# Performance work log

Hardware: AMD Instinct MI355X
Metric: run time of the kernel (lower is better)

The kernel has to match this reference:

```python
import jax, jax.numpy as jnp
import numpy as np

B, L, D = 8, 4096, 768
EPS = 1e-5


def layer_norm(x, g, b):
    mu = jnp.mean(x, axis=-1, keepdims=True)
    var = jnp.mean(jnp.square(x - mu), axis=-1, keepdims=True)
    return (x - mu) * jax.lax.rsqrt(var + EPS) * g + b


def conv1d_same(x_blc, w_oik, b_o):
    # x_blc: [B, L, C] -> torch Conv1d(C, C, 3, padding=1) on [B, C, L]
    x_ncw = jnp.swapaxes(x_blc, 1, 2)
    y = jax.lax.conv_general_dilated(
        x_ncw, w_oik, window_strides=(1,), padding=[(1, 1)],
        dimension_numbers=("NCW", "OIW", "NCW"))
    y = y + b_o[None, :, None]
    return jnp.swapaxes(y, 1, 2)


def simple_ssm(u, a_p, b_p, c_p, d_p):
    # Diagonal SSM: h_t = sigmoid(a)*h_{t-1} + b*u_t ; y_t = c*h_t + d*u_t
    a = jax.nn.sigmoid(a_p)  # [D]

    def step(h, ut):  # h, ut: [B, D]
        h = a * h + b_p * ut
        return h, c_p * h

    h0 = jnp.zeros((u.shape[0], u.shape[2]), u.dtype)
    _, y = jax.lax.scan(step, h0, jnp.swapaxes(u, 0, 1))  # y: [L, B, D]
    return jnp.swapaxes(y, 0, 1) + d_p * u


def setup_inputs() -> dict:
    key = jax.random.key(0)
    ks = jax.random.split(key, 16)
    s_lin = 1.0 / np.sqrt(D)
    s_conv = 1.0 / np.sqrt(3 * D)
    return {
        "x": jax.random.normal(ks[0], (B, L, D), jnp.float32),
        "ln_g": jnp.ones((D,), jnp.float32),
        "ln_b": jnp.zeros((D,), jnp.float32),
        "Wi": jax.random.normal(ks[1], (D, 2 * D), jnp.float32) * s_lin,
        "bi": jnp.zeros((2 * D,), jnp.float32),
        "Wf_conv": jax.random.normal(ks[2], (D, D, 3), jnp.float32) * s_conv,
        "bf_conv": jnp.zeros((D,), jnp.float32),
        "af": jax.random.normal(ks[3], (D,), jnp.float32),
        "bf": jax.random.normal(ks[4], (D,), jnp.float32) * 0.5,
        "cf": jax.random.normal(ks[5], (D,), jnp.float32) * 0.5,
        "df": jax.random.normal(ks[6], (D,), jnp.float32) * 0.5,
        "Wb_conv": jax.random.normal(ks[7], (D, D, 3), jnp.float32) * s_conv,
        "bb_conv": jnp.zeros((D,), jnp.float32),
        "ab": jax.random.normal(ks[8], (D,), jnp.float32),
        "bb": jax.random.normal(ks[9], (D,), jnp.float32) * 0.5,
        "cb": jax.random.normal(ks[10], (D,), jnp.float32) * 0.5,
        "db": jax.random.normal(ks[11], (D,), jnp.float32) * 0.5,
        "Wo": jax.random.normal(ks[12], (D, D), jnp.float32) * s_lin,
        "bo": jnp.zeros((D,), jnp.float32),
    }


def reference(x, ln_g, ln_b, Wi, bi, Wf_conv, bf_conv, af, bf, cf, df,
              Wb_conv, bb_conv, ab, bb, cb, db, Wo, bo):
    residual = x
    xn = layer_norm(x, ln_g, ln_b)
    proj = xn @ Wi + bi                      # [B, L, 2D]
    xg, z = proj[..., :D], proj[..., D:]
    # forward branch
    f = conv1d_same(xg, Wf_conv, bf_conv)
    f = simple_ssm(f, af, bf, cf, df)
    # backward branch (flip along sequence)
    b_in = jnp.flip(xg, axis=1)
    bb_out = conv1d_same(b_in, Wb_conv, bb_conv)
    bb_out = simple_ssm(bb_out, ab, bb, cb, db)
    bb_out = jnp.flip(bb_out, axis=1)
    zg = jax.nn.silu(z)
    y = f * zg + bb_out * zg
    return y @ Wo + bo + residual
```

## Files before the change

### kernel.cpp

```cpp
#include <hip/hip_runtime.h>
#include <cstdint>
#include <cstddef>
#include <math.h>

#define L_SEQ 4096
#define D_DIM 768
#define B_SZ 8
#define M_ROWS (B_SZ * L_SEQ)
#define CHUNK 64

typedef __bf16 bf16x8 __attribute__((ext_vector_type(8)));
typedef float floatx4 __attribute__((ext_vector_type(4)));

#define GLP(p)  ((__attribute__((address_space(1))) const void*)(const void*)(p))
#define LDSP(p) ((__attribute__((address_space(3))) void*)(void*)(p))

__global__ __launch_bounds__(256) void ln_kernel(const float* __restrict__ x,
                                                 const float* __restrict__ g,
                                                 const float* __restrict__ b,
                                                 __bf16* __restrict__ xn) {
  __shared__ float red[256];
  const int tid = threadIdx.x;
  const size_t row = blockIdx.x;
  const float* xr = x + row * D_DIM;
  float v0 = xr[tid];
  float v1 = xr[tid + 256];
  float v2 = xr[tid + 512];
  red[tid] = v0 + v1 + v2;
  __syncthreads();
  for (int off = 128; off > 0; off >>= 1) {
    if (tid < off) red[tid] += red[tid + off];
    __syncthreads();
  }
  float mu = red[0] * (1.0f / D_DIM);
  __syncthreads();
  float d0 = v0 - mu, d1 = v1 - mu, d2 = v2 - mu;
  red[tid] = d0 * d0 + d1 * d1 + d2 * d2;
  __syncthreads();
  for (int off = 128; off > 0; off >>= 1) {
    if (tid < off) red[tid] += red[tid + off];
    __syncthreads();
  }
  float rs = rsqrtf(red[0] * (1.0f / D_DIM) + 1e-5f);
  __bf16* xo = xn + row * D_DIM;
  xo[tid]       = (__bf16)(d0 * rs * g[tid]       + b[tid]);
  xo[tid + 256] = (__bf16)(d1 * rs * g[tid + 256] + b[tid + 256]);
  xo[tid + 512] = (__bf16)(d2 * rs * g[tid + 512] + b[tid + 512]);
}

template<int MODE>
__global__ __launch_bounds__(256) void gemm_kernel(
    const __bf16* __restrict__ A,
    const __bf16* __restrict__ Bt,
    const float* __restrict__ bias,
    const float* __restrict__ resid,
    __bf16* __restrict__ out0,
    __bf16* __restrict__ out1,
    float* __restrict__ outf,
    const __bf16* __restrict__ zbuf,
    int K) {
  __shared__ __bf16 As[128 * 32];
  __shared__ __bf16 Bs[128 * 32];
  const int tid   = threadIdx.x;
  const int tileN = blockIdx.x;
  const int tileM = blockIdx.y;
  const int lane = tid & 63;
  const int w    = tid >> 6;
  const int wm   = w >> 1;
  const int wn   = w & 1;
  const int l15  = lane & 15;
  const int quad = lane >> 4;
  const int colg = (lane & 3) * 8;
  const int rsub = lane >> 2;

  const int rowA0 = w * 32 + rsub;
  const int rowA1 = rowA0 + 16;

  const __bf16* gB0 = Bt + (size_t)(tileN * 128 + rowA0) * K + colg;
  const __bf16* gB1 = Bt + (size_t)(tileN * 128 + rowA1) * K + colg;

  const __bf16* gA0 = nullptr;
  const __bf16* gA1 = nullptr;
  int bl0 = 0, bl1 = 0, l0 = 0, l1 = 0;
  if (MODE == 1 || MODE == 2) {
    int gr0 = tileM * 128 + rowA0;
    int gr1 = tileM * 128 + rowA1;
    bl0 = gr0 >> 12; l0 = gr0 & (L_SEQ - 1);
    bl1 = gr1 >> 12; l1 = gr1 & (L_SEQ - 1);
  } else {
    gA0 = A + (size_t)(tileM * 128 + rowA0) * K + colg;
    gA1 = A + (size_t)(tileM * 128 + rowA1) * K + colg;
  }

  __bf16* ldsA0 = &As[(w * 32) * 32];
  __bf16* ldsA1 = &As[(w * 32 + 16) * 32];
  __bf16* ldsB0 = &Bs[(w * 32) * 32];
  __bf16* ldsB1 = &Bs[(w * 32 + 16) * 32];

  floatx4 acc[4][4];
#pragma unroll
  for (int i = 0; i < 4; ++i)
#pragma unroll
    for (int j = 0; j < 4; ++j)
#pragma unroll
      for (int r = 0; r < 4; ++r) acc[i][j][r] = 0.0f;

  int kblk = 0, i0 = 0;
  for (int kt = 0; kt < K; kt += 32) {
    __syncthreads();
    const __bf16* pa0;
    const __bf16* pa1;
    if (MODE == 1 || MODE == 2) {
      int ls0 = (MODE == 1) ? (l0 + kblk - 1) : (L_SEQ - l0 - kblk);
      int ls1 = (MODE == 1) ? (l1 + kblk - 1) : (L_SEQ - l1 - kblk);
      pa0 = (ls0 >= 0 && ls0 < L_SEQ)
          ? A + ((size_t)(bl0 << 12) + (size_t)ls0) * D_DIM + i0 + colg : zbuf;
      pa1 = (ls1 >= 0 && ls1 < L_SEQ)
          ? A + ((size_t)(bl1 << 12) + (size_t)ls1) * D_DIM + i0 + colg : zbuf;
    } else {
      pa0 = gA0 + kt;
      pa1 = gA1 + kt;
    }
    __builtin_amdgcn_global_load_lds(GLP(pa0), LDSP(ldsA0), 16, 0, 0);
    __builtin_amdgcn_global_load_lds(GLP(pa1), LDSP(ldsA1), 16, 0, 0);
    __builtin_amdgcn_global_load_lds(GLP(gB0 + kt), LDSP(ldsB0), 16, 0, 0);
    __builtin_amdgcn_global_load_lds(GLP(gB1 + kt), LDSP(ldsB1), 16, 0, 0);
    __syncthreads();

    bf16x8 afr[4], bfr[4];
#pragma unroll
    for (int i = 0; i < 4; ++i)
      afr[i] = *(const bf16x8*)(&As[(wm * 64 + i * 16 + l15) * 32 + quad * 8]);
#pragma unroll
    for (int j = 0; j < 4; ++j)
      bfr[j] = *(const bf16x8*)(&Bs[(wn * 64 + j * 16 + l15) * 32 + quad * 8]);
#pragma unroll
    for (int i = 0; i < 4; ++i)
#pragma unroll
      for (int j = 0; j < 4; ++j)
        acc[i][j] = __builtin_amdgcn_mfma_f32_16x16x32_bf16(afr[i], bfr[j], acc[i][j], 0, 0, 0);

    i0 += 32;
    if (i0 == D_DIM) { i0 = 0; ++kblk; }
  }

#pragma unroll
  for (int i = 0; i < 4; ++i) {
#pragma unroll
    for (int j = 0; j < 4; ++j) {
#pragma unroll
      for (int r = 0; r < 4; ++r) {
        int row = tileM * 128 + wm * 64 + i * 16 + quad * 4 + r;
        int col = tileN * 128 + wn * 64 + j * 16 + l15;
        float v = acc[i][j][r] + bias[col];
        if (MODE == 0) {
          if (col < D_DIM) {
            out0[(size_t)row * D_DIM + col] = (__bf16)v;
          } else {
            float s = v / (1.0f + expf(-v));
            out1[(size_t)row * D_DIM + (col - D_DIM)] = (__bf16)s;
          }
        } else if (MODE == 3) {
          size_t o = (size_t)row * D_DIM + col;
          outf[o] = v + resid[o];
        } else {
          out0[(size_t)row * D_DIM + col] = (__bf16)v;
        }
      }
    }
  }
}

__global__ __launch_bounds__(256) void scan1_kernel(
    const float* __restrict__ ap0, const float* __restrict__ bp0,
    const float* __restrict__ ap1, const float* __restrict__ bp1,
    const __bf16* __restrict__ u0, const __bf16* __restrict__ u1,
    float* __restrict__ hl) {
  int idx = blockIdx.x * 256 + threadIdx.x;
  int d = idx % D_DIM;
  int rest = idx / D_DIM;
  int chunk = rest & 63;
  int tb = rest >> 6;
  int b = tb & 7;
  int tensor = tb >> 3;
  const float* ap = tensor ? ap1 : ap0;
  const float* bp = tensor ? bp1 : bp0;
  const __bf16* u = (tensor ? u1 : u0) +
      ((size_t)(b * L_SEQ + chunk * CHUNK)) * D_DIM + d;
  float a  = 1.0f / (1.0f + expf(-ap[d]));
  float bb = bp[d];
  float h = 0.0f;
  for (int t = 0; t < CHUNK; ++t) {
    h = a * h + bb * (float)u[(size_t)t * D_DIM];
  }
  hl[(size_t)idx] = h;
}

__global__ __launch_bounds__(256) void scan2_kernel(
    const float* __restrict__ ap0, const float* __restrict__ ap1,
    float* __restrict__ hl) {
  int idx = blockIdx.x * 256 + threadIdx.x;
  int d = idx % D_DIM;
  int tb = idx / D_DIM;
  int tensor = tb >> 3;
  const float* ap = tensor ? ap1 : ap0;
  float a = 1.0f / (1.0f + expf(-ap[d]));
  float aT = a * a;  aT = aT * aT;  aT = aT * aT;
  aT = aT * aT;      aT = aT * aT;  aT = aT * aT;
  float* base = hl + (size_t)tb * 64 * D_DIM + d;
  float carry = 0.0f;
  for (int c = 0; c < 64; ++c) {
    float* p = base + (size_t)c * D_DIM;
    float tmp = *p;
    *p = carry;
    carry = aT * carry + tmp;
  }
}

__global__ __launch_bounds__(256) void scan3_kernel(
    const float* __restrict__ ap0, const float* __restrict__ bp0,
    const float* __restrict__ cp0, const float* __restrict__ dp0,
    const float* __restrict__ ap1, const float* __restrict__ bp1,
    const float* __restrict__ cp1, const float* __restrict__ dp1,
    __bf16* __restrict__ u0, __bf16* __restrict__ u1,
    const float* __restrict__ hl) {
  int idx = blockIdx.x * 256 + threadIdx.x;
  int d = idx % D_DIM;
  int rest = idx / D_DIM;
  int chunk = rest & 63;
  int tb = rest >> 6;
  int b = tb & 7;
  int tensor = tb >> 3;
  const float* ap = tensor ? ap1 : ap0;
  const float* bp = tensor ? bp1 : bp0;
  const float* cp = tensor ? cp1 : cp0;
  const float* dp = tensor ? dp1 : dp0;
  __bf16* u = (tensor ? u1 : u0) +
      ((size_t)(b * L_SEQ + chunk * CHUNK)) * D_DIM + d;
  float a  = 1.0f / (1.0f + expf(-ap[d]));
  float bb = bp[d];
  float cc = cp[d];
  float dd = dp[d];
  float h = hl[(size_t)idx];
  for (int t = 0; t < CHUNK; ++t) {
    float uv = (float)u[(size_t)t * D_DIM];
    h = a * h + bb * uv;
    u[(size_t)t * D_DIM] = (__bf16)(cc * h + dd * uv);
  }
}

__global__ __launch_bounds__(256) void gate_kernel(const __bf16* __restrict__ f,
                                                   const __bf16* __restrict__ bbuf,
                                                   const __bf16* __restrict__ zg,
                                                   __bf16* __restrict__ y) {
  size_t idx = (size_t)blockIdx.x * 256 + threadIdx.x;
  int d = (int)(idx % D_DIM);
  size_t rl = idx / D_DIM;
  int l = (int)(rl & (L_SEQ - 1));
  size_t b = rl >> 12;
  size_t src = ((b << 12) + (size_t)(L_SEQ - 1 - l)) * D_DIM + d;
  float v = ((float)f[idx] + (float)bbuf[src]) * (float)zg[idx];
  y[idx] = (__bf16)v;
}

__global__ __launch_bounds__(256) void tr_kernel(const float* __restrict__ in,
                                                 __bf16* __restrict__ out,
                                                 int Kdim, int Ndim) {
  int idx = blockIdx.x * 256 + threadIdx.x;
  if (idx >= Kdim * Ndim) return;
  int n = idx / Kdim;
  int k = idx - n * Kdim;
  out[idx] = (__bf16)in[(size_t)k * Ndim + n];
}

__global__ __launch_bounds__(256) void trconv_kernel(const float* __restrict__ in,
                                                     __bf16* __restrict__ out) {
  int idx = blockIdx.x * 256 + threadIdx.x;
  if (idx >= D_DIM * 2304) return;
  int o = idx / 2304;
  int rem = idx - o * 2304;
  int k = rem / D_DIM;
  int i = rem - k * D_DIM;
  out[idx] = (__bf16)in[(size_t)o * 2304 + i * 3 + k];
}

__global__ void zero_kernel(__bf16* z) { z[threadIdx.x] = (__bf16)0.0f; }

extern "C" void kernel_launch(void* const* d_in, const int* in_sizes, int n_in,
                              void* d_out, int out_size, void* d_ws, size_t ws_size,
                              hipStream_t stream) {
  const float* x    = (const float*)d_in[0];
  const float* ln_g = (const float*)d_in[1];
  const float* ln_b = (const float*)d_in[2];
  const float* Wi   = (const float*)d_in[3];
  const float* bi   = (const float*)d_in[4];
  const float* Wf   = (const float*)d_in[5];
  const float* bfc  = (const float*)d_in[6];
  const float* af   = (const float*)d_in[7];
  const float* bfp  = (const float*)d_in[8];
  const float* cfp  = (const float*)d_in[9];
  const float* dfp  = (const float*)d_in[10];
  const float* Wb   = (const float*)d_in[11];
  const float* bbc  = (const float*)d_in[12];
  const float* ab   = (const float*)d_in[13];
  const float* bbp  = (const float*)d_in[14];
  const float* cbp  = (const float*)d_in[15];
  const float* dbp  = (const float*)d_in[16];
  const float* Wo   = (const float*)d_in[17];
  const float* bo   = (const float*)d_in[18];
  float* out = (float*)d_out;

  char* ws = (char*)d_ws;
  const size_t BLD = (size_t)B_SZ * L_SEQ * D_DIM;
  __bf16* ws0 = (__bf16*)(ws);
  __bf16* ws1 = (__bf16*)(ws + BLD * 2);
  __bf16* ws2 = (__bf16*)(ws + BLD * 4);
  __bf16* ws3 = (__bf16*)(ws + BLD * 6);
  __bf16* wit = (__bf16*)(ws + BLD * 8);
  __bf16* wft = wit + (size_t)1536 * 768;
  __bf16* wbt = wft + (size_t)768 * 2304;
  __bf16* wot = wbt + (size_t)768 * 2304;
  __bf16* zbuf = wot + (size_t)768 * 768;
  float* hl = (float*)(ws + BLD * 2);
  const size_t needed = BLD * 8 +
      ((size_t)1536 * 768 + 2 * (size_t)768 * 2304 + (size_t)768 * 768) * 2 + 256;
  if (ws_size < needed) return;

  zero_kernel<<<1, 128, 0, stream>>>(zbuf);
  tr_kernel<<<(768 * 1536 + 255) / 256, 256, 0, stream>>>(Wi, wit, 768, 1536);
  trconv_kernel<<<(768 * 2304 + 255) / 256, 256, 0, stream>>>(Wf, wft);
  trconv_kernel<<<(768 * 2304 + 255) / 256, 256, 0, stream>>>(Wb, wbt);
  tr_kernel<<<(768 * 768 + 255) / 256, 256, 0, stream>>>(Wo, wot, 768, 768);

  ln_kernel<<<M_ROWS, 256, 0, stream>>>(x, ln_g, ln_b, ws0);

  gemm_kernel<0><<<dim3(1536 / 128, M_ROWS / 128), 256, 0, stream>>>(
      ws0, wit, bi, nullptr, ws1, ws2, nullptr, zbuf, 768);

  gemm_kernel<1><<<dim3(768 / 128, M_ROWS / 128), 256, 0, stream>>>(
      ws1, wft, bfc, nullptr, ws0, nullptr, nullptr, zbuf, 2304);
  gemm_kernel<2><<<dim3(768 / 128, M_ROWS / 128), 256, 0, stream>>>(
      ws1, wbt, bbc, nullptr, ws3, nullptr, nullptr, zbuf, 2304);

  {
    const int n1 = 2 * B_SZ * 64 * D_DIM;
    scan1_kernel<<<n1 / 256, 256, 0, stream>>>(af, bfp, ab, bbp, ws0, ws3, hl);
    const int n2 = 2 * B_SZ * D_DIM;
    scan2_kernel<<<n2 / 256, 256, 0, stream>>>(af, ab, hl);
    scan3_kernel<<<n1 / 256, 256, 0, stream>>>(af, bfp, cfp, dfp,
                                               ab, bbp, cbp, dbp,
                                               ws0, ws3, hl);
  }

  gate_kernel<<<(unsigned)(BLD / 256), 256, 0, stream>>>(ws0, ws3, ws2, ws1);

  gemm_kernel<3><<<dim3(768 / 128, M_ROWS / 128), 256, 0, stream>>>(
      ws1, wot, bo, x, nullptr, nullptr, out, zbuf, 768);
}
```

Measured before the change: 879.6 us.

## Replace GEMMs with 256x256 pipelined kernel, merge conv branches, vectorize scans

```diff
diff --git a/kernel.cpp b/kernel.cpp
--- a/kernel.cpp
+++ b/kernel.cpp
@@ -48,123 +48,195 @@
   xo[tid + 512] = (__bf16)(d2 * rs * g[tid + 512] + b[tid + 512]);
 }
 
-template<int MODE>
-__global__ __launch_bounds__(256) void gemm_kernel(
-    const __bf16* __restrict__ A,
-    const __bf16* __restrict__ Bt,
-    const float* __restrict__ bias,
+
+#define VMW(n) asm volatile("s_waitcnt vmcnt(" #n ")" ::: "memory")
+#define BARR   asm volatile("s_barrier" ::: "memory")
+#define MF(a, b, c) __builtin_amdgcn_mfma_f32_16x16x32_bf16((a), (b), (c), 0, 0, 0)
+#define LDV(off) (*(const bf16x8*)(smem + (off)))
+
+#define RDA(BUF, MOFF) do { \
+  aR0k0 = LDV((BUF)*65536 + aoff + (MOFF) + ck0);        aR0k1 = LDV((BUF)*65536 + aoff + (MOFF) + ck1); \
+  aR1k0 = LDV((BUF)*65536 + aoff + (MOFF) + 2048 + ck0); aR1k1 = LDV((BUF)*65536 + aoff + (MOFF) + 2048 + ck1); \
+  aR2k0 = LDV((BUF)*65536 + aoff + (MOFF) + 4096 + ck0); aR2k1 = LDV((BUF)*65536 + aoff + (MOFF) + 4096 + ck1); \
+  aR3k0 = LDV((BUF)*65536 + aoff + (MOFF) + 6144 + ck0); aR3k1 = LDV((BUF)*65536 + aoff + (MOFF) + 6144 + ck1); \
+} while (0)
+
+#define RDB01(BUF) do { \
+  bN0k0 = LDV((BUF)*65536 + boff + ck0);        bN0k1 = LDV((BUF)*65536 + boff + ck1); \
+  bN1k0 = LDV((BUF)*65536 + boff + 2048 + ck0); bN1k1 = LDV((BUF)*65536 + boff + 2048 + ck1); \
+} while (0)
+
+#define RDB23(BUF) do { \
+  bN2k0 = LDV((BUF)*65536 + boff + 4096 + ck0); bN2k1 = LDV((BUF)*65536 + boff + 4096 + ck1); \
+  bN3k0 = LDV((BUF)*65536 + boff + 6144 + ck0); bN3k1 = LDV((BUF)*65536 + boff + 6144 + ck1); \
+} while (0)
+
+#define MMQ01(AI) do { \
+  acc[(AI)+0][0] = MF(aR0k0, bN0k0, acc[(AI)+0][0]); acc[(AI)+0][0] = MF(aR0k1, bN0k1, acc[(AI)+0][0]); \
+  acc[(AI)+0][1] = MF(aR0k0, bN1k0, acc[(AI)+0][1]); acc[(AI)+0][1] = MF(aR0k1, bN1k1, acc[(AI)+0][1]); \
+  acc[(AI)+1][0] = MF(aR1k0, bN0k0, acc[(AI)+1][0]); acc[(AI)+1][0] = MF(aR1k1, bN0k1, acc[(AI)+1][0]); \
+  acc[(AI)+1][1] = MF(aR1k0, bN1k0, acc[(AI)+1][1]); acc[(AI)+1][1] = MF(aR1k1, bN1k1, acc[(AI)+1][1]); \
+  acc[(AI)+2][0] = MF(aR2k0, bN0k0, acc[(AI)+2][0]); acc[(AI)+2][0] = MF(aR2k1, bN0k1, acc[(AI)+2][0]); \
+  acc[(AI)+2][1] = MF(aR2k0, bN1k0, acc[(AI)+2][1]); acc[(AI)+2][1] = MF(aR2k1, bN1k1, acc[(AI)+2][1]); \
+  acc[(AI)+3][0] = MF(aR3k0, bN0k0, acc[(AI)+3][0]); acc[(AI)+3][0] = MF(aR3k1, bN0k1, acc[(AI)+3][0]); \
+  acc[(AI)+3][1] = MF(aR3k0, bN1k0, acc[(AI)+3][1]); acc[(AI)+3][1] = MF(aR3k1, bN1k1, acc[(AI)+3][1]); \
+} while (0)
+
+#define MMQ23(AI) do { \
+  acc[(AI)+0][2] = MF(aR0k0, bN2k0, acc[(AI)+0][2]); acc[(AI)+0][2] = MF(aR0k1, bN2k1, acc[(AI)+0][2]); \
+  acc[(AI)+0][3] = MF(aR0k0, bN3k0, acc[(AI)+0][3]); acc[(AI)+0][3] = MF(aR0k1, bN3k1, acc[(AI)+0][3]); \
+  acc[(AI)+1][2] = MF(aR1k0, bN2k0, acc[(AI)+1][2]); acc[(AI)+1][2] = MF(aR1k1, bN2k1, acc[(AI)+1][2]); \
+  acc[(AI)+1][3] = MF(aR1k0, bN3k0, acc[(AI)+1][3]); acc[(AI)+1][3] = MF(aR1k1, bN3k1, acc[(AI)+1][3]); \
+  acc[(AI)+2][2] = MF(aR2k0, bN2k0, acc[(AI)+2][2]); acc[(AI)+2][2] = MF(aR2k1, bN2k1, acc[(AI)+2][2]); \
+  acc[(AI)+2][3] = MF(aR2k0, bN3k0, acc[(AI)+2][3]); acc[(AI)+2][3] = MF(aR2k1, bN3k1, acc[(AI)+2][3]); \
+  acc[(AI)+3][2] = MF(aR3k0, bN2k0, acc[(AI)+3][2]); acc[(AI)+3][2] = MF(aR3k1, bN2k1, acc[(AI)+3][2]); \
+  acc[(AI)+3][3] = MF(aR3k0, bN3k0, acc[(AI)+3][3]); acc[(AI)+3][3] = MF(aR3k1, bN3k1, acc[(AI)+3][3]); \
+} while (0)
+
+#define STAGE_A_HP(h, p, tkt, BUF) do { \
+  const __bf16* _s; \
+  if (MODE == 1) { \
+    const int _kb = ((tkt) * 43) >> 9;                        \
+    const int _io = (((tkt) - _kb * 12) << 6) + (_kb - 1) * D_DIM; \
+    _s = ((unsigned)(lv##h##p + _kb - 1) < (unsigned)L_SEQ) ? (rb##h##p + _io) : zbuf; \
+  } else { \
+    _s = rb##h##p + (tkt) * 64; \
+  } \
+  __builtin_amdgcn_global_load_lds(GLP(_s), \
+      LDSP(smem + (BUF)*65536 + (h)*8192 + (p)*16384 + dstw), 16, 0, 0); \
+} while (0)
+
+#define STAGE_B_HP(h, p, tkt, BUF) \
+  __builtin_amdgcn_global_load_lds(GLP(pB##h##p + (tkt) * 64), \
+      LDSP(smem + (BUF)*65536 + 32768 + (h)*16384 + (p)*8192 + dstw), 16, 0, 0)
+
+#define TILE(T, BUF, VA, VC, SA1, SREST) do { \
+   \
+  VMW(VA); BARR; \
+  RDB01(BUF); RDA(BUF, 0); \
+  if (SA1) { STAGE_A_HP(1, 0, (T) + 1, (BUF) ^ 1); STAGE_A_HP(1, 1, (T) + 1, (BUF) ^ 1); } \
+  __builtin_amdgcn_s_setprio(1); MMQ01(0); __builtin_amdgcn_s_setprio(0); \
+   \
+  BARR; \
+  RDB23(BUF); \
+  if (SREST) { STAGE_A_HP(0, 0, (T) + 2, (BUF)); STAGE_A_HP(0, 1, (T) + 2, (BUF)); } \
+  __builtin_amdgcn_s_setprio(1); MMQ23(0); __builtin_amdgcn_s_setprio(0); \
+   \
+  VMW(VC); BARR; \
+  RDA(BUF, 8192); \
+  if (SREST) { STAGE_B_HP(0, 0, (T) + 2, (BUF)); STAGE_B_HP(0, 1, (T) + 2, (BUF)); } \
+  __builtin_amdgcn_s_setprio(1); MMQ01(4); __builtin_amdgcn_s_setprio(0); \
+   \
+  if (SREST) { STAGE_B_HP(1, 0, (T) + 2, (BUF)); STAGE_B_HP(1, 1, (T) + 2, (BUF)); } \
+  __builtin_amdgcn_s_setprio(1); MMQ23(4); __builtin_amdgcn_s_setprio(0); \
+} while (0)
+
+template<int MODE, int NT, int NN>
+__global__ __launch_bounds__(512) void gemm256_kernel(
+    const __bf16* __restrict__ A, const __bf16* __restrict__ Bt,
+    const float* __restrict__ bias_lo, const float* __restrict__ bias_hi,
     const float* __restrict__ resid,
-    __bf16* __restrict__ out0,
-    __bf16* __restrict__ out1,
-    float* __restrict__ outf,
-    const __bf16* __restrict__ zbuf,
-    int K) {
-  __shared__ __bf16 As[128 * 32];
-  __shared__ __bf16 Bs[128 * 32];
-  const int tid   = threadIdx.x;
-  const int tileN = blockIdx.x;
-  const int tileM = blockIdx.y;
+    __bf16* __restrict__ out0, __bf16* __restrict__ out1,
+    float* __restrict__ outf, const __bf16* __restrict__ zbuf) {
+  extern __shared__ char smem[];
+  constexpr int K = NT * 64;
+  constexpr int nwg = NN * (M_ROWS / 256);
+  constexpr int cpx = nwg / 8;
+  const int bid = blockIdx.x;
+  const int wgs = (bid & 7) * cpx + (bid >> 3);
+  const int tileN = wgs % NN;
+  const int tileM = wgs / NN;
+  const int tid  = (int)threadIdx.x;
+  const int w    = tid >> 6;
   const int lane = tid & 63;
-  const int w    = tid >> 6;
-  const int wm   = w >> 1;
-  const int wn   = w & 1;
   const int l15  = lane & 15;
   const int quad = lane >> 4;
-  const int colg = (lane & 3) * 8;
-  const int rsub = lane >> 2;
-
-  const int rowA0 = w * 32 + rsub;
-  const int rowA1 = rowA0 + 16;
-
-  const __bf16* gB0 = Bt + (size_t)(tileN * 128 + rowA0) * K + colg;
-  const __bf16* gB1 = Bt + (size_t)(tileN * 128 + rowA1) * K + colg;
-
-  const __bf16* gA0 = nullptr;
-  const __bf16* gA1 = nullptr;
-  int bl0 = 0, bl1 = 0, l0 = 0, l1 = 0;
-  if (MODE == 1 || MODE == 2) {
-    int gr0 = tileM * 128 + rowA0;
-    int gr1 = tileM * 128 + rowA1;
-    bl0 = gr0 >> 12; l0 = gr0 & (L_SEQ - 1);
-    bl1 = gr1 >> 12; l1 = gr1 & (L_SEQ - 1);
-  } else {
-    gA0 = A + (size_t)(tileM * 128 + rowA0) * K + colg;
-    gA1 = A + (size_t)(tileM * 128 + rowA1) * K + colg;
-  }
-
-  __bf16* ldsA0 = &As[(w * 32) * 32];
-  __bf16* ldsA1 = &As[(w * 32 + 16) * 32];
-  __bf16* ldsB0 = &Bs[(w * 32) * 32];
-  __bf16* ldsB1 = &Bs[(w * 32 + 16) * 32];
-
-  floatx4 acc[4][4];
-#pragma unroll
-  for (int i = 0; i < 4; ++i)
+  const int wm   = w >> 2;
+  const int wn   = w & 3;
+
+  const int srow = tid >> 3;
+  const int ce   = ((tid & 7) ^ (srow & 7)) << 3;
+  const int dstw = w << 10;
+
+  const int aoff = (wm * 128 + l15) * 128;
+  const int boff = 32768 + (wn * 64 + l15) * 128;
+  const int ck0  = (quad ^ (l15 & 7)) << 4;
+  const int ck1  = ((4 | quad) ^ (l15 & 7)) << 4;
+
+  const __bf16* pB00 = Bt + (size_t)(tileN * 256 + srow) * K + ce;
+  const __bf16* pB01 = Bt + (size_t)(tileN * 256 + 64 + srow) * K + ce;
+  const __bf16* pB10 = Bt + (size_t)(tileN * 256 + 128 + srow) * K + ce;
+  const __bf16* pB11 = Bt + (size_t)(tileN * 256 + 192 + srow) * K + ce;
+
+  const __bf16 *rb00, *rb01, *rb10, *rb11;
+  int lv00 = 0, lv01 = 0, lv10 = 0, lv11 = 0;
+  {
+    const int g00 = tileM * 256 + srow;
+    const int g01 = tileM * 256 + 128 + srow;
+    const int g10 = tileM * 256 + 64 + srow;
+    const int g11 = tileM * 256 + 192 + srow;
+    if (MODE == 1) {
+      rb00 = A + (size_t)g00 * D_DIM + ce; lv00 = g00 & (L_SEQ - 1);
+      rb01 = A + (size_t)g01 * D_DIM + ce; lv01 = g01 & (L_SEQ - 1);
+      rb10 = A + (size_t)g10 * D_DIM + ce; lv10 = g10 & (L_SEQ - 1);
+      rb11 = A + (size_t)g11 * D_DIM + ce; lv11 = g11 & (L_SEQ - 1);
+    } else {
+      rb00 = A + (size_t)g00 * K + ce;
+      rb01 = A + (size_t)g01 * K + ce;
+      rb10 = A + (size_t)g10 * K + ce;
+      rb11 = A + (size_t)g11 * K + ce;
+    }
+  }
+
+  bf16x8 aR0k0, aR0k1, aR1k0, aR1k1, aR2k0, aR2k1, aR3k0, aR3k1;
+  bf16x8 bN0k0, bN0k1, bN1k0, bN1k1, bN2k0, bN2k1, bN3k0, bN3k1;
+  floatx4 acc[8][4];
+#pragma unroll
+  for (int i = 0; i < 8; ++i)
 #pragma unroll
     for (int j = 0; j < 4; ++j)
 #pragma unroll
       for (int r = 0; r < 4; ++r) acc[i][j][r] = 0.0f;
 
-  int kblk = 0, i0 = 0;
-  for (int kt = 0; kt < K; kt += 32) {
-    __syncthreads();
-    const __bf16* pa0;
-    const __bf16* pa1;
-    if (MODE == 1 || MODE == 2) {
-      int ls0 = (MODE == 1) ? (l0 + kblk - 1) : (L_SEQ - l0 - kblk);
-      int ls1 = (MODE == 1) ? (l1 + kblk - 1) : (L_SEQ - l1 - kblk);
-      pa0 = (ls0 >= 0 && ls0 < L_SEQ)
-          ? A + ((size_t)(bl0 << 12) + (size_t)ls0) * D_DIM + i0 + colg : zbuf;
-      pa1 = (ls1 >= 0 && ls1 < L_SEQ)
-          ? A + ((size_t)(bl1 << 12) + (size_t)ls1) * D_DIM + i0 + colg : zbuf;
-    } else {
-      pa0 = gA0 + kt;
-      pa1 = gA1 + kt;
-    }
-    __builtin_amdgcn_global_load_lds(GLP(pa0), LDSP(ldsA0), 16, 0, 0);
-    __builtin_amdgcn_global_load_lds(GLP(pa1), LDSP(ldsA1), 16, 0, 0);
-    __builtin_amdgcn_global_load_lds(GLP(gB0 + kt), LDSP(ldsB0), 16, 0, 0);
-    __builtin_amdgcn_global_load_lds(GLP(gB1 + kt), LDSP(ldsB1), 16, 0, 0);
-    __syncthreads();
-
-    bf16x8 afr[4], bfr[4];
-#pragma unroll
-    for (int i = 0; i < 4; ++i)
-      afr[i] = *(const bf16x8*)(&As[(wm * 64 + i * 16 + l15) * 32 + quad * 8]);
-#pragma unroll
-    for (int j = 0; j < 4; ++j)
-      bfr[j] = *(const bf16x8*)(&Bs[(wn * 64 + j * 16 + l15) * 32 + quad * 8]);
-#pragma unroll
-    for (int i = 0; i < 4; ++i)
-#pragma unroll
-      for (int j = 0; j < 4; ++j)
-        acc[i][j] = __builtin_amdgcn_mfma_f32_16x16x32_bf16(afr[i], bfr[j], acc[i][j], 0, 0, 0);
-
-    i0 += 32;
-    if (i0 == D_DIM) { i0 = 0; ++kblk; }
-  }
-
-#pragma unroll
-  for (int i = 0; i < 4; ++i) {
-#pragma unroll
-    for (int j = 0; j < 4; ++j) {
+  STAGE_A_HP(0, 0, 0, 0); STAGE_A_HP(0, 1, 0, 0);
+  STAGE_B_HP(0, 0, 0, 0); STAGE_B_HP(0, 1, 0, 0);
+  STAGE_B_HP(1, 0, 0, 0); STAGE_B_HP(1, 1, 0, 0);
+  STAGE_A_HP(1, 0, 0, 0); STAGE_A_HP(1, 1, 0, 0);
+  STAGE_A_HP(0, 0, 1, 1); STAGE_A_HP(0, 1, 1, 1);
+  STAGE_B_HP(0, 0, 1, 1); STAGE_B_HP(0, 1, 1, 1);
+  STAGE_B_HP(1, 0, 1, 1); STAGE_B_HP(1, 1, 1, 1);
+
+  for (int it = 0; it < (NT - 2) / 2; ++it) {
+    const int T0 = it * 2;
+    TILE(T0,     0, 8, 10, 1, 1);
+    TILE(T0 + 1, 1, 8, 10, 1, 1);
+  }
+  TILE(NT - 2, 0, 8, 8, 1, 0);
+  TILE(NT - 1, 1, 2, 0, 0, 0);
+
+  const int rowb = tileM * 256 + wm * 128 + quad * 4;
+  const int colb = tileN * 256 + wn * 64 + l15;
+#pragma unroll
+  for (int mi = 0; mi < 8; ++mi) {
+#pragma unroll
+    for (int nj = 0; nj < 4; ++nj) {
+      const int col = colb + nj * 16;
+      float bv;
+      if (MODE == 3) bv = bias_lo[col];
+      else bv = (col < D_DIM) ? bias_lo[col] : bias_hi[col - D_DIM];
 #pragma unroll
       for (int r = 0; r < 4; ++r) {
-        int row = tileM * 128 + wm * 64 + i * 16 + quad * 4 + r;
-        int col = tileN * 128 + wn * 64 + j * 16 + l15;
-        float v = acc[i][j][r] + bias[col];
-        if (MODE == 0) {
-          if (col < D_DIM) {
-            out0[(size_t)row * D_DIM + col] = (__bf16)v;
-          } else {
-            float s = v / (1.0f + expf(-v));
-            out1[(size_t)row * D_DIM + (col - D_DIM)] = (__bf16)s;
-          }
-        } else if (MODE == 3) {
-          size_t o = (size_t)row * D_DIM + col;
+        const int row = rowb + mi * 16 + r;
+        float v = acc[mi][nj][r] + bv;
+        if (MODE == 3) {
+          const size_t o = (size_t)row * D_DIM + col;
           outf[o] = v + resid[o];
+        } else if (MODE == 0) {
+          if (col < D_DIM) out0[(size_t)row * D_DIM + col] = (__bf16)v;
+          else out1[(size_t)row * D_DIM + (col - D_DIM)] = (__bf16)(v / (1.0f + expf(-v)));
         } else {
-          out0[(size_t)row * D_DIM + col] = (__bf16)v;
+          if (col < D_DIM) out0[(size_t)row * D_DIM + col] = (__bf16)v;
+          else out1[(size_t)row * D_DIM + (col - D_DIM)] = (__bf16)v;
         }
       }
     }
@@ -177,23 +249,33 @@
     const __bf16* __restrict__ u0, const __bf16* __restrict__ u1,
     float* __restrict__ hl) {
   int idx = blockIdx.x * 256 + threadIdx.x;
-  int d = idx % D_DIM;
-  int rest = idx / D_DIM;
+  int dg = idx % 96;
+  int rest = idx / 96;
   int chunk = rest & 63;
   int tb = rest >> 6;
+  int tensor = tb >> 3;
   int b = tb & 7;
-  int tensor = tb >> 3;
-  const float* ap = tensor ? ap1 : ap0;
-  const float* bp = tensor ? bp1 : bp0;
+  const float* ap = (tensor ? ap1 : ap0) + dg * 8;
+  const float* bp = (tensor ? bp1 : bp0) + dg * 8;
   const __bf16* u = (tensor ? u1 : u0) +
-      ((size_t)(b * L_SEQ + chunk * CHUNK)) * D_DIM + d;
-  float a  = 1.0f / (1.0f + expf(-ap[d]));
-  float bb = bp[d];
-  float h = 0.0f;
+      ((size_t)(b * L_SEQ + chunk * CHUNK + (tensor ? CHUNK - 1 : 0))) * D_DIM + dg * 8;
+  const int st = tensor ? -D_DIM : D_DIM;
+  float a[8], bb[8], h[8];
+#pragma unroll
+  for (int j = 0; j < 8; ++j) {
+    a[j] = 1.0f / (1.0f + expf(-ap[j]));
+    bb[j] = bp[j];
+    h[j] = 0.0f;
+  }
   for (int t = 0; t < CHUNK; ++t) {
-    h = a * h + bb * (float)u[(size_t)t * D_DIM];
-  }
-  hl[(size_t)idx] = h;
+    bf16x8 uv = *(const bf16x8*)u;
+#pragma unroll
+    for (int j = 0; j < 8; ++j) h[j] = a[j] * h[j] + bb[j] * (float)uv[j];
+    u += st;
+  }
+  float* o = hl + (size_t)(tb * 64 + chunk) * D_DIM + dg * 8;
+#pragma unroll
+  for (int j = 0; j < 8; ++j) o[j] = h[j];
 }
 
 __global__ __launch_bounds__(256) void scan2_kernel(
@@ -205,15 +287,15 @@
   int tensor = tb >> 3;
   const float* ap = tensor ? ap1 : ap0;
   float a = 1.0f / (1.0f + expf(-ap[d]));
-  float aT = a * a;  aT = aT * aT;  aT = aT * aT;
-  aT = aT * aT;      aT = aT * aT;  aT = aT * aT;
-  float* base = hl + (size_t)tb * 64 * D_DIM + d;
+  float aT = a * a;  aT *= aT;  aT *= aT;  aT *= aT;  aT *= aT;  aT *= aT;
+  float* p = hl + (size_t)tb * 64 * D_DIM + d + (tensor ? 63 * D_DIM : 0);
+  const int st = tensor ? -D_DIM : D_DIM;
   float carry = 0.0f;
   for (int c = 0; c < 64; ++c) {
-    float* p = base + (size_t)c * D_DIM;
     float tmp = *p;
     *p = carry;
     carry = aT * carry + tmp;
+    p += st;
   }
 }
 
@@ -225,27 +307,38 @@
     __bf16* __restrict__ u0, __bf16* __restrict__ u1,
     const float* __restrict__ hl) {
   int idx = blockIdx.x * 256 + threadIdx.x;
-  int d = idx % D_DIM;
-  int rest = idx / D_DIM;
+  int dg = idx % 96;
+  int rest = idx / 96;
   int chunk = rest & 63;
   int tb = rest >> 6;
+  int tensor = tb >> 3;
   int b = tb & 7;
-  int tensor = tb >> 3;
-  const float* ap = tensor ? ap1 : ap0;
-  const float* bp = tensor ? bp1 : bp0;
-  const float* cp = tensor ? cp1 : cp0;
-  const float* dp = tensor ? dp1 : dp0;
+  const float* ap = (tensor ? ap1 : ap0) + dg * 8;
+  const float* bp = (tensor ? bp1 : bp0) + dg * 8;
+  const float* cp = (tensor ? cp1 : cp0) + dg * 8;
+  const float* dp = (tensor ? dp1 : dp0) + dg * 8;
   __bf16* u = (tensor ? u1 : u0) +
-      ((size_t)(b * L_SEQ + chunk * CHUNK)) * D_DIM + d;
-  float a  = 1.0f / (1.0f + expf(-ap[d]));
-  float bb = bp[d];
-  float cc = cp[d];
-  float dd = dp[d];
-  float h = hl[(size_t)idx];
+      ((size_t)(b * L_SEQ + chunk * CHUNK + (tensor ? CHUNK - 1 : 0))) * D_DIM + dg * 8;
+  const int st = tensor ? -D_DIM : D_DIM;
+  const float* hp = hl + (size_t)(tb * 64 + chunk) * D_DIM + dg * 8;
+  float a[8], bb[8], cc[8], dd[8], h[8];
+#pragma unroll
+  for (int j = 0; j < 8; ++j) {
+    a[j] = 1.0f / (1.0f + expf(-ap[j]));
+    bb[j] = bp[j]; cc[j] = cp[j]; dd[j] = dp[j];
+    h[j] = hp[j];
+  }
   for (int t = 0; t < CHUNK; ++t) {
-    float uv = (float)u[(size_t)t * D_DIM];
-    h = a * h + bb * uv;
-    u[(size_t)t * D_DIM] = (__bf16)(cc * h + dd * uv);
+    bf16x8 uv = *(const bf16x8*)u;
+    bf16x8 ov;
+#pragma unroll
+    for (int j = 0; j < 8; ++j) {
+      float xv = (float)uv[j];
+      h[j] = a[j] * h[j] + bb[j] * xv;
+      ov[j] = (__bf16)(cc[j] * h[j] + dd[j] * xv);
+    }
+    *(bf16x8*)u = ov;
+    u += st;
   }
 }
 
@@ -253,14 +346,15 @@
                                                    const __bf16* __restrict__ bbuf,
                                                    const __bf16* __restrict__ zg,
                                                    __bf16* __restrict__ y) {
-  size_t idx = (size_t)blockIdx.x * 256 + threadIdx.x;
-  int d = (int)(idx % D_DIM);
-  size_t rl = idx / D_DIM;
-  int l = (int)(rl & (L_SEQ - 1));
-  size_t b = rl >> 12;
-  size_t src = ((b << 12) + (size_t)(L_SEQ - 1 - l)) * D_DIM + d;
-  float v = ((float)f[idx] + (float)bbuf[src]) * (float)zg[idx];
-  y[idx] = (__bf16)v;
+  size_t e = ((size_t)blockIdx.x * 256 + threadIdx.x) * 8;
+  bf16x8 f8 = *(const bf16x8*)(f + e);
+  bf16x8 b8 = *(const bf16x8*)(bbuf + e);
+  bf16x8 z8 = *(const bf16x8*)(zg + e);
+  bf16x8 o;
+#pragma unroll
+  for (int j = 0; j < 8; ++j)
+    o[j] = (__bf16)(((float)f8[j] + (float)b8[j]) * (float)z8[j]);
+  *(bf16x8*)(y + e) = o;
 }
 
 __global__ __launch_bounds__(256) void tr_kernel(const float* __restrict__ in,
@@ -274,14 +368,16 @@
 }
 
 __global__ __launch_bounds__(256) void trconv_kernel(const float* __restrict__ in,
-                                                     __bf16* __restrict__ out) {
+                                                     __bf16* __restrict__ out,
+                                                     int rev) {
   int idx = blockIdx.x * 256 + threadIdx.x;
   if (idx >= D_DIM * 2304) return;
   int o = idx / 2304;
   int rem = idx - o * 2304;
   int k = rem / D_DIM;
   int i = rem - k * D_DIM;
-  out[idx] = (__bf16)in[(size_t)o * 2304 + i * 3 + k];
+  int ks = rev ? (2 - k) : k;
+  out[idx] = (__bf16)in[(size_t)o * 2304 + i * 3 + ks];
 }
 
 __global__ void zero_kernel(__bf16* z) { z[threadIdx.x] = (__bf16)0.0f; }
@@ -316,44 +412,46 @@
   __bf16* ws1 = (__bf16*)(ws + BLD * 2);
   __bf16* ws2 = (__bf16*)(ws + BLD * 4);
   __bf16* ws3 = (__bf16*)(ws + BLD * 6);
-  __bf16* wit = (__bf16*)(ws + BLD * 8);
-  __bf16* wft = wit + (size_t)1536 * 768;
-  __bf16* wbt = wft + (size_t)768 * 2304;
-  __bf16* wot = wbt + (size_t)768 * 2304;
+  __bf16* wit  = (__bf16*)(ws + BLD * 8);
+  __bf16* wcat = wit + (size_t)1536 * 768;
+  __bf16* wot  = wcat + (size_t)1536 * 2304;
   __bf16* zbuf = wot + (size_t)768 * 768;
   float* hl = (float*)(ws + BLD * 2);
   const size_t needed = BLD * 8 +
-      ((size_t)1536 * 768 + 2 * (size_t)768 * 2304 + (size_t)768 * 768) * 2 + 256;
+      ((size_t)1536 * 768 + (size_t)1536 * 2304 + (size_t)768 * 768) * 2 + 256;
   if (ws_size < needed) return;
+
+  static bool attr_done = false;
+  if (!attr_done) {
+    (void)hipFuncSetAttribute(reinterpret_cast<const void*>(&gemm256_kernel<0, 12, 6>),
+                              hipFuncAttributeMaxDynamicSharedMemorySize, 131072);
+    (void)hipFuncSetAttribute(reinterpret_cast<const void*>(&gemm256_kernel<1, 36, 6>),
+                              hipFuncAttributeMaxDynamicSharedMemorySize, 131072);
+    (void)hipFuncSetAttribute(reinterpret_cast<const void*>(&gemm256_kernel<3, 12, 3>),
+                              hipFuncAttributeMaxDynamicSharedMemorySize, 131072);
+    attr_done = true;
+  }
 
   zero_kernel<<<1, 128, 0, stream>>>(zbuf);
   tr_kernel<<<(768 * 1536 + 255) / 256, 256, 0, stream>>>(Wi, wit, 768, 1536);
-  trconv_kernel<<<(768 * 2304 + 255) / 256, 256, 0, stream>>>(Wf, wft);
-  trconv_kernel<<<(768 * 2304 + 255) / 256, 256, 0, stream>>>(Wb, wbt);
+  trconv_kernel<<<(768 * 2304 + 255) / 256, 256, 0, stream>>>(Wf, wcat, 0);
+  trconv_kernel<<<(768 * 2304 + 255) / 256, 256, 0, stream>>>(Wb, wcat + (size_t)768 * 2304, 1);
   tr_kernel<<<(768 * 768 + 255) / 256, 256, 0, stream>>>(Wo, wot, 768, 768);
 
   ln_kernel<<<M_ROWS, 256, 0, stream>>>(x, ln_g, ln_b, ws0);
 
-  gemm_kernel<0><<<dim3(1536 / 128, M_ROWS / 128), 256, 0, stream>>>(
-      ws0, wit, bi, nullptr, ws1, ws2, nullptr, zbuf, 768);
-
-  gemm_kernel<1><<<dim3(768 / 128, M_ROWS / 128), 256, 0, stream>>>(
-      ws1, wft, bfc, nullptr, ws0, nullptr, nullptr, zbuf, 2304);
-  gemm_kernel<2><<<dim3(768 / 128, M_ROWS / 128), 256, 0, stream>>>(
-      ws1, wbt, bbc, nullptr, ws3, nullptr, nullptr, zbuf, 2304);
-
-  {
-    const int n1 = 2 * B_SZ * 64 * D_DIM;
-    scan1_kernel<<<n1 / 256, 256, 0, stream>>>(af, bfp, ab, bbp, ws0, ws3, hl);
-    const int n2 = 2 * B_SZ * D_DIM;
-    scan2_kernel<<<n2 / 256, 256, 0, stream>>>(af, ab, hl);
-    scan3_kernel<<<n1 / 256, 256, 0, stream>>>(af, bfp, cfp, dfp,
-                                               ab, bbp, cbp, dbp,
-                                               ws0, ws3, hl);
-  }
-
-  gate_kernel<<<(unsigned)(BLD / 256), 256, 0, stream>>>(ws0, ws3, ws2, ws1);
-
-  gemm_kernel<3><<<dim3(768 / 128, M_ROWS / 128), 256, 0, stream>>>(
-      ws1, wot, bo, x, nullptr, nullptr, out, zbuf, 768);
-}
+  gemm256_kernel<0, 12, 6><<<768, 512, 131072, stream>>>(
+      ws0, wit, bi, bi + 768, nullptr, ws1, ws2, nullptr, zbuf);
+
+  gemm256_kernel<1, 36, 6><<<768, 512, 131072, stream>>>(
+      ws1, wcat, bfc, bbc, nullptr, ws0, ws3, nullptr, zbuf);
+
+  scan1_kernel<<<384, 256, 0, stream>>>(af, bfp, ab, bbp, ws0, ws3, hl);
+  scan2_kernel<<<48, 256, 0, stream>>>(af, ab, hl);
+  scan3_kernel<<<384, 256, 0, stream>>>(af, bfp, cfp, dfp, ab, bbp, cbp, dbp, ws0, ws3, hl);
+
+  gate_kernel<<<12288, 256, 0, stream>>>(ws0, ws3, ws2, ws1);
+
+  gemm256_kernel<3, 12, 3><<<384, 512, 131072, stream>>>(
+      ws1, wot, bo, bo, x, nullptr, nullptr, out, zbuf);
+}
```

Result: faster. 746.4 us (-15.1%).
